# Optimization experiments

Hardware: AMD Instinct MI355X
Metric: run time of the kernel (lower is better)

Reference implementation:

```python
import jax, jax.numpy as jnp
import numpy as np

TAU = 3.0          # CPG tau
VTH = 1.0          # LIF v_threshold (v_reset = 0, hard reset)
PEAK = 16          # peak population size
NUM_E = 25         # int(32 * 0.8) excitatory neurons
FATIGUE_TH = 8
ALPHA = 4.0        # spikingjelly sigmoid surrogate alpha (unused in fwd)


def spike_fn(x):
    # Heaviside threshold at 0 (v >= VTH fires)
    return (x >= 0.0).astype(x.dtype)


def setup_inputs() -> dict:
    key = jax.random.key(0)
    k0, k1, k2, k3, k4 = jax.random.split(key, 5)
    B, N = 524288, 32
    spike_history = (jax.random.uniform(k0, (B, N)) < 0.3).astype(jnp.float32)
    neighbor_E_spikes = (jax.random.uniform(k1, (B, 8, NUM_E)) < 0.3).astype(jnp.float32)
    # mutual_inhibition: -2.0 everywhere, within-population blocks *0.1 -> -0.2,
    # cross-population blocks set to -3.0
    is_peak = jnp.arange(N) < PEAK
    same_pop = is_peak[:, None] == is_peak[None, :]
    mutual_inhibition = jnp.where(same_pop, -0.2, -3.0).astype(jnp.float32)
    coupling_W = jax.random.normal(k2, (N, NUM_E), dtype=jnp.float32) * 0.2
    peak_fatigue = jax.random.randint(k3, (B,), 0, 10, dtype=jnp.int32)
    trough_fatigue = jax.random.randint(k4, (B,), 0, 10, dtype=jnp.int32)
    v0 = jnp.zeros((B, N), dtype=jnp.float32)
    return {
        "spike_history": spike_history,
        "neighbor_E_spikes": neighbor_E_spikes,
        "mutual_inhibition": mutual_inhibition,
        "coupling_W": coupling_W,
        "v0": v0,
        "peak_fatigue": peak_fatigue,
        "trough_fatigue": trough_fatigue,
        "num_ticks": 5,
    }


def reference(spike_history, neighbor_E_spikes, mutual_inhibition, coupling_W,
              v0, peak_fatigue, trough_fatigue, num_ticks):
    B = spike_history.shape[0]
    # fatigue-driven drive: trough fatigue excites peak half, peak fatigue excites trough half
    dp = jnp.where(trough_fatigue >= FATIGUE_TH, 2.0, 0.0)[:, None]  # [B,1]
    dt = jnp.where(peak_fatigue >= FATIGUE_TH, 2.0, 0.0)[:, None]
    drive = jnp.concatenate(
        [jnp.broadcast_to(dp, (B, PEAK)), jnp.broadcast_to(dt, (B, 32 - PEAK))], axis=-1)
    # neighbor coupling: sum_k W @ nbr_k ; constant across ticks, hoisted out of loop
    coupling = jnp.einsum('bkn,mn->bm', neighbor_E_spikes, coupling_W)
    base = drive + 0.3 * coupling  # [B,32]

    def step(carry, _):
        v, sh, acc = carry
        recurrent = jnp.einsum('bn,mn->bm', sh, mutual_inhibition)  # sh @ M.T
        x = base + 0.5 * recurrent
        # LIF (decay_input=True): v += (x - (v - v_reset)) / tau, v_reset = 0
        v = v + (x - v) / TAU
        s = spike_fn(v - VTH)
        v = v * (1.0 - s)  # hard reset to 0
        return (v, s, acc + s), None

    init = (v0, spike_history, jnp.zeros_like(v0))
    (v, sh, acc), _ = jax.lax.scan(step, init, None, length=num_ticks)
    should_stay = acc[:, PEAK:].sum(axis=-1) > 0.5  # trough active => STAY
    return acc[:, :NUM_E], should_stay
```

## Files before the change

kernel.cpp:

```cpp
#include <hip/hip_runtime.h>


#define FATIGUE_TH 8

__global__ __launch_bounds__(256) void AgentLSM_70841190580507_kernel(
    const float* __restrict__ sh_in,
    const float* __restrict__ nbr,
    const float* __restrict__ M,
    const float* __restrict__ W,
    const int*   __restrict__ pf,
    const int*   __restrict__ tf,
    const int*   __restrict__ ticks_p,
    float* __restrict__ out_acc,
    float* __restrict__ out_stay,
    int B)
{
    __shared__ float4 lds_W4[200];
    __shared__ float4 lds_nbr4[400];
    __shared__ float  lds_cnt[8 * 26];
    __shared__ float  lds_out[200];
    __shared__ float  lds_stay[8];

    const int tid = threadIdx.x;
    const int w   = tid >> 6;
    const int l   = tid & 63;
    const int g   = tid >> 5;
    const int m   = tid & 31;
    const long long b = (long long)blockIdx.x * 8 + g;
    const bool valid = (b < (long long)B);

    if (tid < 200) lds_W4[tid] = ((const float4*)W)[tid];
    __syncthreads();

    const float4* nb4 = (const float4*)nbr;
    const long long cbase = (long long)blockIdx.x * 400 + w * 100;
    const long long ctot  = (long long)B * 50;
    const float4 z = make_float4(0.f, 0.f, 0.f, 0.f);
    {
        long long c0 = cbase + l;
        lds_nbr4[w * 100 + l] = (c0 < ctot) ? nb4[c0] : z;
        if (l < 36) {
            long long c1 = cbase + 64 + l;
            lds_nbr4[w * 100 + 64 + l] = (c1 < ctot) ? nb4[c1] : z;
        }
    }

    float drive = 0.f;
    int init_bit = 0;
    if (valid) {
        drive = (m < 16) ? ((tf[b] >= FATIGUE_TH) ? 2.0f : 0.0f)
                         : ((pf[b] >= FATIGUE_TH) ? 2.0f : 0.0f);
        init_bit = (sh_in[b * 32 + m] != 0.0f);
    }
    const float a_same  = M[0];
    const float a_cross = M[16];
    const int T = ticks_p[0];

    const float* lds_nbr = (const float*)lds_nbr4;
    if (m < 25) {
        float c = 0.f;
        #pragma unroll
        for (int k = 0; k < 8; ++k) c += lds_nbr[g * 200 + k * 25 + m];
        lds_cnt[g * 26 + m] = c;
    }

    const float* lds_W = (const float*)lds_W4;
    float coup = 0.f;
    #pragma unroll
    for (int n = 0; n < 25; ++n)
        coup += lds_cnt[g * 26 + n] * lds_W[m * 25 + n];

    float base = drive + 0.3f * coup;
    float v = 0.0f;

    unsigned long long bal = __ballot(init_bit);
    unsigned int mask = (unsigned int)(bal >> (tid & 32));

    int acc = 0;
    unsigned int any_tr = 0;
    const bool is_peak = (m < 16);

    #define TICK()  do {                                                   \
        float Spf = (float)__popc(mask & 0xFFFFu);                         \
        float Stf = (float)__popc(mask >> 16);                             \
        float rec = is_peak ? (a_same * Spf + a_cross * Stf)               \
                            : (a_cross * Spf + a_same * Stf);              \
        float x = base + 0.5f * rec;                                       \
        v = v + (x - v) / 3.0f;                  \
        bool s = (v >= 1.0f);                 \
        unsigned long long sb = __ballot(s);                               \
        mask = (unsigned int)(sb >> (tid & 32));                           \
        any_tr |= (mask >> 16);                                            \
        acc += s ? 1 : 0;                                                  \
        v = s ? 0.0f : v;                                                  \
    } while (0)

    if (T == 5) {
        TICK(); TICK(); TICK(); TICK(); TICK();
    } else {
        for (int t = 0; t < T; ++t) TICK();
    }
    #undef TICK

    if (m < 25) lds_out[g * 25 + m] = (float)acc;
    if (m == 31) lds_stay[g] = any_tr ? 1.0f : 0.0f;

    const long long obase = (long long)blockIdx.x * 200 + w * 50;
    if (l < 50) {
        long long o = obase + l;
        if (o < (long long)B * 25) out_acc[o] = lds_out[w * 50 + l];
    } else if (l < 52) {
        long long sbi = (long long)blockIdx.x * 8 + w * 2 + (l - 50);
        if (sbi < (long long)B) out_stay[sbi] = lds_stay[w * 2 + (l - 50)];
    }
}

extern "C" void kernel_launch(void* const* d_in, const int* in_sizes, int n_in,
                              void* d_out, int out_size, void* d_ws, size_t ws_size,
                              hipStream_t stream) {
    const float* sh    = (const float*)d_in[0];
    const float* nbr   = (const float*)d_in[1];
    const float* M     = (const float*)d_in[2];
    const float* W     = (const float*)d_in[3];
    const int*   pf    = (const int*)d_in[5];
    const int*   tf    = (const int*)d_in[6];
    const int*   ticks = (const int*)d_in[7];

    const int B = in_sizes[5];
    float* out_acc  = (float*)d_out;
    float* out_stay = out_acc + (long long)B * 25;

    const int blocks = (B + 7) / 8;
    AgentLSM_70841190580507_kernel<<<blocks, 256, 0, stream>>>(
        sh, nbr, M, W, pf, tf, ticks, out_acc, out_stay, B);
}
```

Baseline: 657.5 us.

## Use persistent grid-stride wavefronts with register prefetch of next agent pair

The kernel becomes a persistent grid-stride loop capped at 4096 blocks. Each wavefront handles two agents per iteration and prefetches the next pair's neighbor spikes, state and fatigue into registers while computing the current pair. W is staged once per block in padded LDS rows so the coupling dot product can use float4 reads. This removes per-block setup cost and overlaps global loads with compute. In exchange, the neighbor loads are now strided scalar reads instead of coalesced float4 loads, and relying on intra-wavefront LDS ordering without barriers is a correctness risk.

Result: no change. 645.9 us (-1.8%).

```diff
diff --git a/kernel.cpp b/kernel.cpp
--- a/kernel.cpp
+++ b/kernel.cpp
@@ -2,6 +2,30 @@
 
 
 #define FATIGUE_TH 8
+
+__device__ __forceinline__ void load_pair(
+    long long p, long long npairs, long long B, int grp, int m,
+    const float* __restrict__ nbr, const float* __restrict__ sh_in,
+    const int* __restrict__ pf, const int* __restrict__ tf,
+    float (&nb)[8], float& shv, float& drive)
+{
+    long long b = 2 * p + grp;
+    bool v = (p < npairs) && (b < B);
+    #pragma unroll
+    for (int k = 0; k < 8; ++k) nb[k] = 0.f;
+    shv = 0.f;
+    drive = 0.f;
+    if (v) {
+        if (m < 25) {
+            const float* q = nbr + b * 200 + m;
+            #pragma unroll
+            for (int k = 0; k < 8; ++k) nb[k] = q[k * 25];
+        }
+        shv = sh_in[b * 32 + m];
+        int src = (m < 16) ? tf[b] : pf[b];
+        drive = (src >= FATIGUE_TH) ? 2.0f : 0.0f;
+    }
+}
 
 __global__ __launch_bounds__(256) void AgentLSM_70841190580507_kernel(
     const float* __restrict__ sh_in,
@@ -15,103 +39,105 @@
     float* __restrict__ out_stay,
     int B)
 {
-    __shared__ float4 lds_W4[200];
-    __shared__ float4 lds_nbr4[400];
-    __shared__ float  lds_cnt[8 * 26];
-    __shared__ float  lds_out[200];
-    __shared__ float  lds_stay[8];
+    __shared__ float lds_W[32 * 28];
+    __shared__ float lds_cnt[8 * 28];
+    __shared__ float lds_out[8 * 25];
 
-    const int tid = threadIdx.x;
-    const int w   = tid >> 6;
-    const int l   = tid & 63;
-    const int g   = tid >> 5;
-    const int m   = tid & 31;
-    const long long b = (long long)blockIdx.x * 8 + g;
-    const bool valid = (b < (long long)B);
+    const int tid  = threadIdx.x;
+    const int w    = tid >> 6;
+    const int l    = tid & 63;
+    const int slot = tid >> 5;
+    const int grp  = slot & 1;
+    const int m    = tid & 31;
 
-    if (tid < 200) lds_W4[tid] = ((const float4*)W)[tid];
+    for (int i = tid; i < 800; i += 256)
+        lds_W[(i / 25) * 28 + (i % 25)] = W[i];
+    if (tid < 32) {
+        lds_W[tid * 28 + 25] = 0.f;
+        lds_W[tid * 28 + 26] = 0.f;
+        lds_W[tid * 28 + 27] = 0.f;
+    }
     __syncthreads();
 
-    const float4* nb4 = (const float4*)nbr;
-    const long long cbase = (long long)blockIdx.x * 400 + w * 100;
-    const long long ctot  = (long long)B * 50;
-    const float4 z = make_float4(0.f, 0.f, 0.f, 0.f);
-    {
-        long long c0 = cbase + l;
-        lds_nbr4[w * 100 + l] = (c0 < ctot) ? nb4[c0] : z;
-        if (l < 36) {
-            long long c1 = cbase + 64 + l;
-            lds_nbr4[w * 100 + 64 + l] = (c1 < ctot) ? nb4[c1] : z;
-        }
-    }
-
-    float drive = 0.f;
-    int init_bit = 0;
-    if (valid) {
-        drive = (m < 16) ? ((tf[b] >= FATIGUE_TH) ? 2.0f : 0.0f)
-                         : ((pf[b] >= FATIGUE_TH) ? 2.0f : 0.0f);
-        init_bit = (sh_in[b * 32 + m] != 0.0f);
-    }
     const float a_same  = M[0];
     const float a_cross = M[16];
-    const int T = ticks_p[0];
+    const int   T       = ticks_p[0];
+    const bool  is_peak = (m < 16);
 
-    const float* lds_nbr = (const float*)lds_nbr4;
-    if (m < 25) {
+    const long long npairs  = ((long long)B + 1) >> 1;
+    const long long wstride = (long long)gridDim.x * 4;
+    long long p = (long long)blockIdx.x * 4 + w;
+
+    float nb[8], shv, drive;
+    load_pair(p, npairs, B, grp, m, nbr, sh_in, pf, tf, nb, shv, drive);
+
+    while (p < npairs) {
+        long long pn = p + wstride;
+        float nb2[8], shv2, drive2;
+        load_pair(pn, npairs, B, grp, m, nbr, sh_in, pf, tf, nb2, shv2, drive2);
+
         float c = 0.f;
         #pragma unroll
-        for (int k = 0; k < 8; ++k) c += lds_nbr[g * 200 + k * 25 + m];
-        lds_cnt[g * 26 + m] = c;
-    }
+        for (int k = 0; k < 8; ++k) c += nb[k];
+        if (m < 28) lds_cnt[slot * 28 + m] = (m < 25) ? c : 0.f;
 
-    const float* lds_W = (const float*)lds_W4;
-    float coup = 0.f;
-    #pragma unroll
-    for (int n = 0; n < 25; ++n)
-        coup += lds_cnt[g * 26 + n] * lds_W[m * 25 + n];
+        float coup = 0.f;
+        const float4* c4p = (const float4*)(lds_cnt + slot * 28);
+        const float4* w4p = (const float4*)(lds_W + m * 28);
+        #pragma unroll
+        for (int j = 0; j < 7; ++j) {
+            float4 c4 = c4p[j];
+            float4 w4 = w4p[j];
+            coup += c4.x * w4.x;
+            coup += c4.y * w4.y;
+            coup += c4.z * w4.z;
+            coup += c4.w * w4.w;
+        }
 
-    float base = drive + 0.3f * coup;
-    float v = 0.0f;
+        float base = drive + 0.3f * coup;
+        float v = 0.0f;
 
-    unsigned long long bal = __ballot(init_bit);
-    unsigned int mask = (unsigned int)(bal >> (tid & 32));
+        unsigned long long bal = __ballot(shv != 0.0f);
+        unsigned int mask = (unsigned int)(bal >> (tid & 32));
 
-    int acc = 0;
-    unsigned int any_tr = 0;
-    const bool is_peak = (m < 16);
+        int acc = 0;
+        unsigned int any_tr = 0;
 
-    #define TICK()  do {                                                   \
-        float Spf = (float)__popc(mask & 0xFFFFu);                         \
-        float Stf = (float)__popc(mask >> 16);                             \
-        float rec = is_peak ? (a_same * Spf + a_cross * Stf)               \
-                            : (a_cross * Spf + a_same * Stf);              \
-        float x = base + 0.5f * rec;                                       \
-        v = v + (x - v) / 3.0f;                  \
-        bool s = (v >= 1.0f);                 \
-        unsigned long long sb = __ballot(s);                               \
-        mask = (unsigned int)(sb >> (tid & 32));                           \
-        any_tr |= (mask >> 16);                                            \
-        acc += s ? 1 : 0;                                                  \
-        v = s ? 0.0f : v;                                                  \
-    } while (0)
+        #define TICK()  do {                                                 \
+            float Spf = (float)__popc(mask & 0xFFFFu);                       \
+            float Stf = (float)__popc(mask >> 16);                           \
+            float rec = is_peak ? (a_same * Spf + a_cross * Stf)             \
+                                : (a_cross * Spf + a_same * Stf);            \
+            float x = base + 0.5f * rec;                                     \
+            v = v + (x - v) / 3.0f;                \
+            bool s = (v >= 1.0f);                                            \
+            unsigned long long sb = __ballot(s);                             \
+            mask = (unsigned int)(sb >> (tid & 32));                         \
+            any_tr |= (mask >> 16);                                          \
+            acc += s ? 1 : 0;                                                \
+            v = s ? 0.0f : v;                                                \
+        } while (0)
 
-    if (T == 5) {
-        TICK(); TICK(); TICK(); TICK(); TICK();
-    } else {
-        for (int t = 0; t < T; ++t) TICK();
-    }
-    #undef TICK
+        if (T == 5) {
+            TICK(); TICK(); TICK(); TICK(); TICK();
+        } else {
+            for (int t = 0; t < T; ++t) TICK();
+        }
+        #undef TICK
 
-    if (m < 25) lds_out[g * 25 + m] = (float)acc;
-    if (m == 31) lds_stay[g] = any_tr ? 1.0f : 0.0f;
+        if (m < 25) lds_out[slot * 25 + m] = (float)acc;
+        long long b = 2 * p + grp;
+        if (m == 31 && b < B) out_stay[b] = any_tr ? 1.0f : 0.0f;
 
-    const long long obase = (long long)blockIdx.x * 200 + w * 50;
-    if (l < 50) {
-        long long o = obase + l;
-        if (o < (long long)B * 25) out_acc[o] = lds_out[w * 50 + l];
-    } else if (l < 52) {
-        long long sbi = (long long)blockIdx.x * 8 + w * 2 + (l - 50);
-        if (sbi < (long long)B) out_stay[sbi] = lds_stay[w * 2 + (l - 50)];
+        long long obase = 2 * p * 25;
+        if (l < 50 && obase + l < (long long)B * 25)
+            out_acc[obase + l] = lds_out[w * 50 + l];
+
+        p = pn;
+        #pragma unroll
+        for (int k = 0; k < 8; ++k) nb[k] = nb2[k];
+        shv = shv2;
+        drive = drive2;
     }
 }
 
@@ -130,7 +156,10 @@
     float* out_acc  = (float*)d_out;
     float* out_stay = out_acc + (long long)B * 25;
 
-    const int blocks = (B + 7) / 8;
+    const long long npairs = ((long long)B + 1) >> 1;
+    int blocks = (int)((npairs + 3) / 4);
+    if (blocks > 4096) blocks = 4096;
+    if (blocks < 1) blocks = 1;
     AgentLSM_70841190580507_kernel<<<blocks, 256, 0, stream>>>(
         sh, nbr, M, W, pf, tf, ticks, out_acc, out_stay, B);
 }
```
